# Kernel tuning notes

Measured on AMD Instinct MI355X. Metric: run time of the kernel, lower is better.

Reference implementation:

```python
import jax, jax.numpy as jnp
import numpy as np

NUM_CELLS = 1  # default num_cells=1 -> 27 periodic image shifts


def _combos(dtype):
    pos = jnp.arange(-NUM_CELLS, NUM_CELLS + 1)
    g = jnp.stack(jnp.meshgrid(pos, pos, pos, indexing='xy'), axis=0)  # [3,3,3,3]
    return g.transpose(3, 2, 1, 0).reshape(-1, 3).astype(dtype)  # [27,3]


def setup_inputs() -> dict:
    key = jax.random.key(0)
    k1, k2, k3 = jax.random.split(key, 3)
    box = 12.0  # Angstrom-scale cubic box, typical for LiPS supercell
    stacked_radii = jax.random.uniform(k1, (2, 4, 512, 3), dtype=jnp.float32) * box
    cell = box * jnp.eye(3, dtype=jnp.float32)
    bonds = jax.random.randint(k2, (768, 2), 0, 512)
    mean_bond_lens = jax.random.uniform(k3, (768,), dtype=jnp.float32) * 0.5 + 1.5
    return {"stacked_radii": stacked_radii, "cell": cell,
            "bonds": bonds, "mean_bond_lens": mean_bond_lens}


def reference(stacked_radii, cell, bonds, mean_bond_lens):
    combos = _combos(cell.dtype)          # [27,3]
    shifts = combos @ cell                # [27,3]; == sum_i cell[i,j]*combos[k,i]

    def dist_mat(coords):                 # coords: [B,N,3]
        shifted = coords[:, :, None, :] + shifts[None, None]     # [B,N,27,3]
        d = coords[:, :, None, None, :] - shifted[:, None]        # [B,N,N,27,3]
        dist = jnp.sqrt(jnp.sum(d * d, axis=-1))                  # [B,N,N,27]
        return jnp.min(dist, axis=-1)                             # [B,N,N]

    dists = jax.vmap(dist_mat)(stacked_radii)                     # [T,B,N,N]
    bond_lens = dists[:, :, bonds[:, 0], bonds[:, 1]]             # [T,B,n_bonds]
    dev = jnp.abs(bond_lens - mean_bond_lens)
    max_bond_dev_per_replica = jax.lax.stop_gradient(dev.max(axis=-1).max(axis=0))  # [B]
    return bond_lens, max_bond_dev_per_replica
```

## Files before the change

### kernel.cpp

```cpp
#include <hip/hip_runtime.h>
#include <hip/hip_bf16.h>


__device__ __forceinline__ float axis_min_sq(float ci, float cj, float box) {
    float d0 = ci - (cj - box);
    float d1 = ci - cj;
    float d2 = ci - (cj + box);
    d0 *= d0; d1 *= d1; d2 *= d2;
    return fminf(d0, fminf(d1, d2));
}

__global__ __launch_bounds__(256) void bond_dev_kernel(
    const float* __restrict__ radii,
    const float* __restrict__ cell,
    const int*   __restrict__ bonds,
    const float* __restrict__ mean,
    float*       __restrict__ out)
{
    const int idx = blockIdx.x * 256 + threadIdx.x;
    const int b = idx % 768;
    const int s = (idx / 768) & 3;
    const int r = idx / 3072;

    const float bx = cell[0];
    const float by = cell[4];
    const float bz = cell[8];

    const int i = bonds[2 * b];
    const int j = bonds[2 * b + 1];

    const float* base = radii + (size_t)((r * 4 + s) * 512) * 3;
    const float xi = base[3 * i], yi = base[3 * i + 1], zi = base[3 * i + 2];
    const float xj = base[3 * j], yj = base[3 * j + 1], zj = base[3 * j + 2];

    const float dsq = axis_min_sq(xi, xj, bx)
                    + axis_min_sq(yi, yj, by)
                    + axis_min_sq(zi, zj, bz);
    const float len = sqrtf(dsq);
    out[idx] = len;

    float v = fabsf(len - mean[b]);

    #pragma unroll
    for (int o = 32; o > 0; o >>= 1)
        v = fmaxf(v, __shfl_down(v, o, 64));

    __shared__ float wmax[4];
    const int lane = threadIdx.x & 63;
    const int wid  = threadIdx.x >> 6;
    if (lane == 0) wmax[wid] = v;
    __syncthreads();

    if (threadIdx.x == 0) {
        const float m = fmaxf(fmaxf(wmax[0], wmax[1]), fmaxf(wmax[2], wmax[3]));
        atomicMax((unsigned int*)(out + 6144 + s), __float_as_uint(m));
    }
}

extern "C" void kernel_launch(void* const* d_in, const int* in_sizes, int n_in,
                              void* d_out, int out_size, void* d_ws, size_t ws_size,
                              hipStream_t stream) {
    const float* radii = (const float*)d_in[0];
    const float* cell  = (const float*)d_in[1];
    const int*   bonds = (const int*)d_in[2];
    const float* mean  = (const float*)d_in[3];
    float* out = (float*)d_out;

    hipMemsetAsync((char*)d_out + 6144 * sizeof(float), 0, 4 * sizeof(float), stream);

    const int total = 2 * 4 * 768;
    bond_dev_kernel<<<total / 256, 256, 0, stream>>>(radii, cell, bonds, mean, out);
}
```

Baseline: 11.32 us.

## Use one block per replica to drop memset and atomics

Each block now owns one replica index and loops over all 768 bonds and both time slices, so the max deviation is reduced inside the block and written directly. This removes the separate hipMemsetAsync launch and the global atomicMax. In exchange the grid shrinks from 24 blocks to 4, so each thread does six bond evaluations serially and far fewer CUs are used.

```diff
diff --git a/kernel.cpp b/kernel.cpp
--- a/kernel.cpp
+++ b/kernel.cpp
@@ -17,44 +17,49 @@
     const float* __restrict__ mean,
     float*       __restrict__ out)
 {
-    const int idx = blockIdx.x * 256 + threadIdx.x;
-    const int b = idx % 768;
-    const int s = (idx / 768) & 3;
-    const int r = idx / 3072;
+    const int s = blockIdx.x;
+    const int t = threadIdx.x;
 
     const float bx = cell[0];
     const float by = cell[4];
     const float bz = cell[8];
 
-    const int i = bonds[2 * b];
-    const int j = bonds[2 * b + 1];
+    float vmax = 0.0f;
 
-    const float* base = radii + (size_t)((r * 4 + s) * 512) * 3;
-    const float xi = base[3 * i], yi = base[3 * i + 1], zi = base[3 * i + 2];
-    const float xj = base[3 * j], yj = base[3 * j + 1], zj = base[3 * j + 2];
+    #pragma unroll
+    for (int k = 0; k < 3; ++k) {
+        const int b = k * 256 + t;
+        const int i = bonds[2 * b];
+        const int j = bonds[2 * b + 1];
+        const float mb = mean[b];
 
-    const float dsq = axis_min_sq(xi, xj, bx)
-                    + axis_min_sq(yi, yj, by)
-                    + axis_min_sq(zi, zj, bz);
-    const float len = sqrtf(dsq);
-    out[idx] = len;
+        #pragma unroll
+        for (int r = 0; r < 2; ++r) {
+            const float* base = radii + (size_t)((r * 4 + s) * 512) * 3;
+            const float xi = base[3 * i], yi = base[3 * i + 1], zi = base[3 * i + 2];
+            const float xj = base[3 * j], yj = base[3 * j + 1], zj = base[3 * j + 2];
 
-    float v = fabsf(len - mean[b]);
+            const float dsq = axis_min_sq(xi, xj, bx)
+                            + axis_min_sq(yi, yj, by)
+                            + axis_min_sq(zi, zj, bz);
+            const float len = sqrtf(dsq);
+            out[(r * 4 + s) * 768 + b] = len;
+            vmax = fmaxf(vmax, fabsf(len - mb));
+        }
+    }
 
     #pragma unroll
     for (int o = 32; o > 0; o >>= 1)
-        v = fmaxf(v, __shfl_down(v, o, 64));
+        vmax = fmaxf(vmax, __shfl_down(vmax, o, 64));
 
     __shared__ float wmax[4];
-    const int lane = threadIdx.x & 63;
-    const int wid  = threadIdx.x >> 6;
-    if (lane == 0) wmax[wid] = v;
+    const int lane = t & 63;
+    const int wid  = t >> 6;
+    if (lane == 0) wmax[wid] = vmax;
     __syncthreads();
 
-    if (threadIdx.x == 0) {
-        const float m = fmaxf(fmaxf(wmax[0], wmax[1]), fmaxf(wmax[2], wmax[3]));
-        atomicMax((unsigned int*)(out + 6144 + s), __float_as_uint(m));
-    }
+    if (t == 0)
+        out[6144 + s] = fmaxf(fmaxf(wmax[0], wmax[1]), fmaxf(wmax[2], wmax[3]));
 }
 
 extern "C" void kernel_launch(void* const* d_in, const int* in_sizes, int n_in,
@@ -66,8 +71,5 @@
     const float* mean  = (const float*)d_in[3];
     float* out = (float*)d_out;
 
-    hipMemsetAsync((char*)d_out + 6144 * sizeof(float), 0, 4 * sizeof(float), stream);
-
-    const int total = 2 * 4 * 768;
-    bond_dev_kernel<<<total / 256, 256, 0, stream>>>(radii, cell, bonds, mean, out);
+    bond_dev_kernel<<<4, 256, 0, stream>>>(radii, cell, bonds, mean, out);
 }
```

New measurement: 9.660 us. -14.7%, faster.
